# Kernel tuning notes

Measured on AMD Instinct MI355X. Metric: run time of the kernel, lower is better.

The kernel has to match this reference:

```python
import jax, jax.numpy as jnp
import numpy as np

N_NODES = 50000
HIDDEN = 128
N_EDGES = 1_600_000


def gcn_conv(x, W, b, src, dst, n_nodes):
    """PyG GCNConv: linear, add self-loops, symmetric deg^-1/2 normalization, scatter-sum."""
    h = x @ W  # [N, D]
    # degree with self-loops: 1 + in-degree from edges (edge weight 1)
    deg = jnp.ones((n_nodes,), h.dtype).at[dst].add(1.0)
    dinv = jax.lax.rsqrt(deg)  # deg^{-1/2}, deg >= 1 so no inf
    # neighbor messages: norm_e = dinv[src] * dinv[dst]
    msgs = h[src] * (dinv[src] * dinv[dst])[:, None]  # [E, D]
    agg = jnp.zeros_like(h).at[dst].add(msgs)
    # self-loop contribution: norm = dinv[i]*dinv[i]
    agg = agg + h * (dinv * dinv)[:, None]
    return agg + b


def setup_inputs() -> dict:
    key = jax.random.key(0)
    ks = jax.random.split(key, 7)
    x = jax.random.normal(ks[0], (N_NODES, HIDDEN), dtype=jnp.float32)
    edge_index = jax.random.randint(ks[1], (2, N_EDGES), 0, N_NODES, dtype=jnp.int64)
    s = 1.0 / np.sqrt(HIDDEN)
    W1 = jax.random.uniform(ks[2], (HIDDEN, HIDDEN), jnp.float32, -s, s)
    b1 = jax.random.uniform(ks[3], (HIDDEN,), jnp.float32, -s, s)
    W2 = jax.random.uniform(ks[4], (HIDDEN, HIDDEN), jnp.float32, -s, s)
    b2 = jax.random.uniform(ks[5], (HIDDEN,), jnp.float32, -s, s)
    return {"x": x, "edge_index": edge_index, "W1": W1, "b1": b1, "W2": W2, "b2": b2}


def reference(x, edge_index, W1, b1, W2, b2):
    src, dst = edge_index[0], edge_index[1]
    h = jax.nn.relu(gcn_conv(x, W1, b1, src, dst, N_NODES))
    z = gcn_conv(h, W2, b2, src, dst, N_NODES)
    return z
```

## Files before the change

kernel.cpp:

```cpp
#include <hip/hip_runtime.h>
#include <hip/hip_fp16.h>
#include <type_traits>

#define D 128
#define NI 128
#define NR 25000


__global__ __launch_bounds__(1024) void histA_kernel(const int* __restrict__ dst,
                                                     int* __restrict__ c,
                                                     int E, int N, int CH) {
  __shared__ int cnt[NR];
  int i = blockIdx.x, r = blockIdx.y;
  int base = r * NR;
  int kmax = min(NR, N - base);
  for (int k = threadIdx.x; k < kmax; k += 1024) cnt[k] = 0;
  __syncthreads();
  int e0 = i * CH, e1 = min(e0 + CH, E);
  for (int e = e0 + (int)threadIdx.x; e < e1; e += 1024) {
    unsigned dr = (unsigned)(dst[e] - base);
    if (dr < (unsigned)kmax) atomicAdd(&cnt[dr], 1);
  }
  __syncthreads();
  int* ci = c + (size_t)i * N + base;
  for (int k = threadIdx.x; k < kmax; k += 1024) ci[k] = cnt[k];
}


__global__ __launch_bounds__(256) void histB_kernel(int* __restrict__ c,
                                                    int* __restrict__ deg, int N) {
  int n = blockIdx.x * 256 + threadIdx.x;
  if (n >= N) return;
  int run = 0;
  #pragma unroll 8
  for (int i = 0; i < NI; ++i) {
    size_t idx = (size_t)i * N + n;
    int v = c[idx];
    c[idx] = run;
    run += v;
  }
  deg[n] = run;
}


__global__ __launch_bounds__(256) void bsum_kernel(const int* __restrict__ deg,
                                                   int* __restrict__ bsum) {
  __shared__ int ws[4];
  int i0 = blockIdx.x * 1024 + threadIdx.x * 4;
  int4 v = *reinterpret_cast<const int4*>(deg + i0);
  int s = v.x + v.y + v.z + v.w;
  #pragma unroll
  for (int off = 32; off; off >>= 1) s += __shfl_down(s, off);
  if ((threadIdx.x & 63) == 0) ws[threadIdx.x >> 6] = s;
  __syncthreads();
  if (threadIdx.x == 0) bsum[blockIdx.x] = ws[0] + ws[1] + ws[2] + ws[3];
}


__global__ __launch_bounds__(256) void scan_kernel(const int* __restrict__ deg,
                                                   const int* __restrict__ bsum,
                                                   int* __restrict__ offsets,
                                                   float* __restrict__ dinv,
                                                   int N, int E) {
  __shared__ int ts[256];
  int b = blockIdx.x;
  int base = 0;
  for (int t = 0; t < b; ++t) base += bsum[t];

  int i0 = b * 1024 + threadIdx.x * 4;
  int4 v = *reinterpret_cast<const int4*>(deg + i0);
  int t4 = v.x + v.y + v.z + v.w;
  ts[threadIdx.x] = t4;
  __syncthreads();
  #pragma unroll
  for (int off = 1; off < 256; off <<= 1) {
    int u = (threadIdx.x >= off) ? ts[threadIdx.x - off] : 0;
    __syncthreads();
    ts[threadIdx.x] += u;
    __syncthreads();
  }
  int run = base + ts[threadIdx.x] - t4;

  int dd[4] = {v.x, v.y, v.z, v.w};
  #pragma unroll
  for (int k = 0; k < 4; ++k) {
    int i = i0 + k;
    if (i < N) {
      offsets[i] = run;
      dinv[i] = rsqrtf(1.0f + (float)dd[k]);
    }
    run += dd[k];
  }
  if (b == 0 && threadIdx.x == 0) offsets[N] = E;
}


__global__ __launch_bounds__(1024) void placeC_kernel(const int* __restrict__ src,
                                                      const int* __restrict__ dst,
                                                      const int* __restrict__ c,
                                                      const int* __restrict__ offsets,
                                                      const float* __restrict__ dinv,
                                                      unsigned int* __restrict__ csr,
                                                      int E, int N, int CH) {
  __shared__ int cnt[NR];
  int i = blockIdx.x, r = blockIdx.y;
  int base = r * NR;
  int kmax = min(NR, N - base);
  const int* ci = c + (size_t)i * N + base;
  for (int k = threadIdx.x; k < kmax; k += 1024) cnt[k] = offsets[base + k] + ci[k];
  __syncthreads();
  int e0 = i * CH, e1 = min(e0 + CH, E);
  for (int e = e0 + (int)threadIdx.x; e < e1; e += 1024) {
    int d = dst[e];
    unsigned dr = (unsigned)(d - base);
    if (dr < (unsigned)kmax) {
      int pos = atomicAdd(&cnt[dr], 1);
      int s = src[e];
      float nm = dinv[s] * dinv[d];
      unsigned int q = (unsigned int)__float2int_rn(nm * 32767.0f);
      csr[pos] = ((unsigned int)s << 15) | q;
    }
  }
}


template <typename TI>
__global__ __launch_bounds__(256) void gemm_kernel(const TI* __restrict__ X,
                                                   const float* __restrict__ W,
                                                   __half* __restrict__ H, int N) {
  __shared__ float xs[32 * D];
  int row0 = blockIdx.x * 32;
  if constexpr (std::is_same<TI, float>::value) {
    #pragma unroll
    for (int jj = 0; jj < 4; ++jj) {
      int f4 = threadIdx.x + jj * 256;
      int r = f4 >> 5;
      float4 v = make_float4(0.f, 0.f, 0.f, 0.f);
      if (row0 + r < N) v = *reinterpret_cast<const float4*>(X + (size_t)row0 * D + (size_t)f4 * 4);
      *reinterpret_cast<float4*>(xs + f4 * 4) = v;
    }
  } else {
    #pragma unroll
    for (int jj = 0; jj < 2; ++jj) {
      int g8 = threadIdx.x + jj * 256;
      int r = g8 >> 4;
      uint4 raw = make_uint4(0u, 0u, 0u, 0u);
      if (row0 + r < N)
        raw = *reinterpret_cast<const uint4*>((const __half*)X + (size_t)row0 * D + (size_t)g8 * 8);
      const __half2* hp = reinterpret_cast<const __half2*>(&raw);
      float* dst8 = xs + (size_t)g8 * 8;
      #pragma unroll
      for (int k = 0; k < 4; ++k) {
        float2 f = __half22float2(hp[k]);
        dst8[k * 2] = f.x;
        dst8[k * 2 + 1] = f.y;
      }
    }
  }
  __syncthreads();

  int tx = threadIdx.x & 63;
  int ty = threadIdx.x >> 6;
  int c0 = tx * 2;
  float2 acc[8];
  #pragma unroll
  for (int r = 0; r < 8; ++r) acc[r] = make_float2(0.f, 0.f);
  const float* xbase = xs + ty * 8 * D;

  for (int k = 0; k < D; k += 4) {
    float2 w0 = *reinterpret_cast<const float2*>(W + (size_t)(k + 0) * D + c0);
    float2 w1 = *reinterpret_cast<const float2*>(W + (size_t)(k + 1) * D + c0);
    float2 w2 = *reinterpret_cast<const float2*>(W + (size_t)(k + 2) * D + c0);
    float2 w3 = *reinterpret_cast<const float2*>(W + (size_t)(k + 3) * D + c0);
    #pragma unroll
    for (int r = 0; r < 8; ++r) {
      float4 xv = *reinterpret_cast<const float4*>(xbase + r * D + k);
      acc[r].x = fmaf(xv.x, w0.x, acc[r].x); acc[r].y = fmaf(xv.x, w0.y, acc[r].y);
      acc[r].x = fmaf(xv.y, w1.x, acc[r].x); acc[r].y = fmaf(xv.y, w1.y, acc[r].y);
      acc[r].x = fmaf(xv.z, w2.x, acc[r].x); acc[r].y = fmaf(xv.z, w2.y, acc[r].y);
      acc[r].x = fmaf(xv.w, w3.x, acc[r].x); acc[r].y = fmaf(xv.w, w3.y, acc[r].y);
    }
  }

  #pragma unroll
  for (int r = 0; r < 8; ++r) {
    int row = row0 + ty * 8 + r;
    if (row < N)
      *reinterpret_cast<__half2*>(H + (size_t)row * D + c0) = __floats2half2_rn(acc[r].x, acc[r].y);
  }
}


template <int DO_RELU, typename TO>
__global__ __launch_bounds__(256) void agg_kernel(const __half* __restrict__ H,
                                                  const int* __restrict__ offsets,
                                                  const unsigned int* __restrict__ csr,
                                                  const float* __restrict__ dinv,
                                                  const float* __restrict__ bias,
                                                  TO* __restrict__ out, int N) {
  int n = blockIdx.x * 4 + (threadIdx.x >> 6);
  if (n >= N) return;
  int lane = threadIdx.x & 63;
  int g = lane >> 4;
  int l = lane & 15;

  int beg = offsets[n];
  int end = offsets[n + 1];

  float acc[8];
  #pragma unroll
  for (int k = 0; k < 8; ++k) acc[k] = 0.f;

  const __half* Hl = H + l * 8;

  int j = beg + g;
  for (; j + 12 < end; j += 16) {
    unsigned int p0 = csr[j];
    unsigned int p1 = csr[j + 4];
    unsigned int p2 = csr[j + 8];
    unsigned int p3 = csr[j + 12];
    float m0 = (float)(p0 & 0x7fffu) * (1.0f / 32767.0f);
    float m1 = (float)(p1 & 0x7fffu) * (1.0f / 32767.0f);
    float m2 = (float)(p2 & 0x7fffu) * (1.0f / 32767.0f);
    float m3 = (float)(p3 & 0x7fffu) * (1.0f / 32767.0f);
    uint4 r0 = *reinterpret_cast<const uint4*>(Hl + (size_t)(p0 >> 15) * D);
    uint4 r1 = *reinterpret_cast<const uint4*>(Hl + (size_t)(p1 >> 15) * D);
    uint4 r2 = *reinterpret_cast<const uint4*>(Hl + (size_t)(p2 >> 15) * D);
    uint4 r3 = *reinterpret_cast<const uint4*>(Hl + (size_t)(p3 >> 15) * D);
    const __half2* h0 = reinterpret_cast<const __half2*>(&r0);
    const __half2* h1 = reinterpret_cast<const __half2*>(&r1);
    const __half2* h2 = reinterpret_cast<const __half2*>(&r2);
    const __half2* h3 = reinterpret_cast<const __half2*>(&r3);
    #pragma unroll
    for (int k = 0; k < 4; ++k) {
      float2 f0 = __half22float2(h0[k]);
      float2 f1 = __half22float2(h1[k]);
      float2 f2 = __half22float2(h2[k]);
      float2 f3 = __half22float2(h3[k]);
      acc[2 * k]     = fmaf(f0.x, m0, acc[2 * k]);
      acc[2 * k + 1] = fmaf(f0.y, m0, acc[2 * k + 1]);
      acc[2 * k]     = fmaf(f1.x, m1, acc[2 * k]);
      acc[2 * k + 1] = fmaf(f1.y, m1, acc[2 * k + 1]);
      acc[2 * k]     = fmaf(f2.x, m2, acc[2 * k]);
      acc[2 * k + 1] = fmaf(f2.y, m2, acc[2 * k + 1]);
      acc[2 * k]     = fmaf(f3.x, m3, acc[2 * k]);
      acc[2 * k + 1] = fmaf(f3.y, m3, acc[2 * k + 1]);
    }
  }
  for (; j < end; j += 4) {
    unsigned int p0 = csr[j];
    float m0 = (float)(p0 & 0x7fffu) * (1.0f / 32767.0f);
    uint4 r0 = *reinterpret_cast<const uint4*>(Hl + (size_t)(p0 >> 15) * D);
    const __half2* h0 = reinterpret_cast<const __half2*>(&r0);
    #pragma unroll
    for (int k = 0; k < 4; ++k) {
      float2 f0 = __half22float2(h0[k]);
      acc[2 * k]     = fmaf(f0.x, m0, acc[2 * k]);
      acc[2 * k + 1] = fmaf(f0.y, m0, acc[2 * k + 1]);
    }
  }

  #pragma unroll
  for (int k = 0; k < 8; ++k) {
    acc[k] += __shfl_xor(acc[k], 16);
    acc[k] += __shfl_xor(acc[k], 32);
  }

  if (g == 0) {
    float di = dinv[n];
    float dii = di * di;
    uint4 rs = *reinterpret_cast<const uint4*>(Hl + (size_t)n * D);
    const __half2* hs = reinterpret_cast<const __half2*>(&rs);
    float4 bv0 = *reinterpret_cast<const float4*>(bias + l * 8);
    float4 bv1 = *reinterpret_cast<const float4*>(bias + l * 8 + 4);
    float v[8];
    #pragma unroll
    for (int k = 0; k < 4; ++k) {
      float2 f = __half22float2(hs[k]);
      v[2 * k]     = fmaf(f.x, dii, acc[2 * k]);
      v[2 * k + 1] = fmaf(f.y, dii, acc[2 * k + 1]);
    }
    v[0] += bv0.x; v[1] += bv0.y; v[2] += bv0.z; v[3] += bv0.w;
    v[4] += bv1.x; v[5] += bv1.y; v[6] += bv1.z; v[7] += bv1.w;
    if (DO_RELU) {
      #pragma unroll
      for (int k = 0; k < 8; ++k) v[k] = fmaxf(v[k], 0.f);
    }
    if constexpr (std::is_same<TO, float>::value) {
      float4 o0 = make_float4(v[0], v[1], v[2], v[3]);
      float4 o1 = make_float4(v[4], v[5], v[6], v[7]);
      *reinterpret_cast<float4*>(out + (size_t)n * D + l * 8) = o0;
      *reinterpret_cast<float4*>(out + (size_t)n * D + l * 8 + 4) = o1;
    } else {
      uint4 pk;
      __half2 q0 = __floats2half2_rn(v[0], v[1]);
      __half2 q1 = __floats2half2_rn(v[2], v[3]);
      __half2 q2 = __floats2half2_rn(v[4], v[5]);
      __half2 q3 = __floats2half2_rn(v[6], v[7]);
      pk.x = *reinterpret_cast<unsigned int*>(&q0);
      pk.y = *reinterpret_cast<unsigned int*>(&q1);
      pk.z = *reinterpret_cast<unsigned int*>(&q2);
      pk.w = *reinterpret_cast<unsigned int*>(&q3);
      *reinterpret_cast<uint4*>((__half*)out + (size_t)n * D + l * 8) = pk;
    }
  }
}


extern "C" void kernel_launch(void* const* d_in, const int* in_sizes, int n_in,
                              void* d_out, int out_size, void* d_ws, size_t ws_size,
                              hipStream_t stream) {
  const float* x  = (const float*)d_in[0];
  const int* edge = (const int*)d_in[1];
  const float* W1 = (const float*)d_in[2];
  const float* b1 = (const float*)d_in[3];
  const float* W2 = (const float*)d_in[4];
  const float* b2 = (const float*)d_in[5];
  const int N = in_sizes[0] / D;
  const int E = in_sizes[1] / 2;
  const int* srcp = edge;
  const int* dstp = edge + E;
  float* out = (float*)d_out;

  const int NP = (N + 1023) & ~1023;
  const int SB = NP / 1024;
  const int CH = (E + NI - 1) / NI;
  const int NRB = (N + NR - 1) / NR;

  auto align = [](size_t v) { return (v + 255) & ~(size_t)255; };
  char* ws = (char*)d_ws;
  size_t o = 0;
  int*   deg     = (int*)(ws + o);             o += align((size_t)NP * 4);
  int*   bsum    = (int*)(ws + o);             o += align((size_t)SB * 4);
  int*   offsets = (int*)(ws + o);             o += align((size_t)(N + 1) * 4);
  float* dinv    = (float*)(ws + o);           o += align((size_t)N * 4);
  int*   c       = (int*)(ws + o);             o += align((size_t)NI * N * 4);
  unsigned int* csr = (unsigned int*)(ws + o); o += align((size_t)E * 4);
  __half* Hh     = (__half*)(ws + o);          o += align((size_t)N * D * 2);
  __half* h1h    = (__half*)(ws + o);          o += align((size_t)N * D * 2);

  int gemm_blocks = (N + 31) / 32;
  int agg_blocks  = (N + 3) / 4;

  hipMemsetAsync(deg, 0, (size_t)NP * 4, stream);
  histA_kernel<<<dim3(NI, NRB), 1024, 0, stream>>>(dstp, c, E, N, CH);
  histB_kernel<<<(N + 255) / 256, 256, 0, stream>>>(c, deg, N);
  bsum_kernel<<<SB, 256, 0, stream>>>(deg, bsum);
  scan_kernel<<<SB, 256, 0, stream>>>(deg, bsum, offsets, dinv, N, E);
  placeC_kernel<<<dim3(NI, NRB), 1024, 0, stream>>>(srcp, dstp, c, offsets, dinv, csr, E, N, CH);

  gemm_kernel<float><<<gemm_blocks, 256, 0, stream>>>(x, W1, Hh, N);
  agg_kernel<1, __half><<<agg_blocks, 256, 0, stream>>>(Hh, offsets, csr, dinv, b1, h1h, N);

  gemm_kernel<__half><<<gemm_blocks, 256, 0, stream>>>(h1h, W2, Hh, N);
  agg_kernel<0, float><<<agg_blocks, 256, 0, stream>>>(Hh, offsets, csr, dinv, b2, out, N);
}
```

Baseline: 241.2 us.

## Use MFMA fp16 GEMM with pre-transposed weights and 16-bit histogram counters

Replaces the scalar-FMA shared-memory GEMM with an MFMA 16x16x32 f16 kernel. Each wave loads its A rows straight into registers and reads a transposed fp16 copy of W, which a small new prep kernel builds. Separately, the per-chunk histogram count array shrinks from int to unsigned short, halving its traffic in histA, histB and placeC. The risks are fp16 rounding of x and W before the multiply, and overflow of the 16-bit prefix counts if a single node has more than 65535 incoming edges.

```diff
diff --git a/kernel.cpp b/kernel.cpp
--- a/kernel.cpp
+++ b/kernel.cpp
@@ -6,9 +6,25 @@
 #define NI 128
 #define NR 25000
 
+using half8 = __attribute__((ext_vector_type(8))) _Float16;
+using f32x4 = __attribute__((ext_vector_type(4))) float;
+
+
+__global__ __launch_bounds__(256) void wprep_kernel(const float* __restrict__ W1,
+                                                    const float* __restrict__ W2,
+                                                    __half* __restrict__ Wt1,
+                                                    __half* __restrict__ Wt2) {
+  const float* W = blockIdx.x ? W2 : W1;
+  __half* Wt = blockIdx.x ? Wt2 : Wt1;
+  for (int idx = threadIdx.x; idx < D * D; idx += 256) {
+    int c = idx & 127, k = idx >> 7;
+    Wt[c * D + k] = __float2half(W[k * D + c]);
+  }
+}
+
 
 __global__ __launch_bounds__(1024) void histA_kernel(const int* __restrict__ dst,
-                                                     int* __restrict__ c,
+                                                     unsigned short* __restrict__ c,
                                                      int E, int N, int CH) {
   __shared__ int cnt[NR];
   int i = blockIdx.x, r = blockIdx.y;
@@ -22,12 +38,12 @@
     if (dr < (unsigned)kmax) atomicAdd(&cnt[dr], 1);
   }
   __syncthreads();
-  int* ci = c + (size_t)i * N + base;
-  for (int k = threadIdx.x; k < kmax; k += 1024) ci[k] = cnt[k];
-}
-
-
-__global__ __launch_bounds__(256) void histB_kernel(int* __restrict__ c,
+  unsigned short* ci = c + (size_t)i * N + base;
+  for (int k = threadIdx.x; k < kmax; k += 1024) ci[k] = (unsigned short)cnt[k];
+}
+
+
+__global__ __launch_bounds__(256) void histB_kernel(unsigned short* __restrict__ c,
                                                     int* __restrict__ deg, int N) {
   int n = blockIdx.x * 256 + threadIdx.x;
   if (n >= N) return;
@@ -36,7 +52,7 @@
   for (int i = 0; i < NI; ++i) {
     size_t idx = (size_t)i * N + n;
     int v = c[idx];
-    c[idx] = run;
+    c[idx] = (unsigned short)run;
     run += v;
   }
   deg[n] = run;
@@ -97,7 +113,7 @@
 
 __global__ __launch_bounds__(1024) void placeC_kernel(const int* __restrict__ src,
                                                       const int* __restrict__ dst,
-                                                      const int* __restrict__ c,
+                                                      const unsigned short* __restrict__ c,
                                                       const int* __restrict__ offsets,
                                                       const float* __restrict__ dinv,
                                                       unsigned int* __restrict__ csr,
@@ -106,8 +122,8 @@
   int i = blockIdx.x, r = blockIdx.y;
   int base = r * NR;
   int kmax = min(NR, N - base);
-  const int* ci = c + (size_t)i * N + base;
-  for (int k = threadIdx.x; k < kmax; k += 1024) cnt[k] = offsets[base + k] + ci[k];
+  const unsigned short* ci = c + (size_t)i * N + base;
+  for (int k = threadIdx.x; k < kmax; k += 1024) cnt[k] = offsets[base + k] + (int)ci[k];
   __syncthreads();
   int e0 = i * CH, e1 = min(e0 + CH, E);
   for (int e = e0 + (int)threadIdx.x; e < e1; e += 1024) {
@@ -125,68 +141,50 @@
 
 
 template <typename TI>
-__global__ __launch_bounds__(256) void gemm_kernel(const TI* __restrict__ X,
-                                                   const float* __restrict__ W,
-                                                   __half* __restrict__ H, int N) {
-  __shared__ float xs[32 * D];
-  int row0 = blockIdx.x * 32;
-  if constexpr (std::is_same<TI, float>::value) {
-    #pragma unroll
-    for (int jj = 0; jj < 4; ++jj) {
-      int f4 = threadIdx.x + jj * 256;
-      int r = f4 >> 5;
-      float4 v = make_float4(0.f, 0.f, 0.f, 0.f);
-      if (row0 + r < N) v = *reinterpret_cast<const float4*>(X + (size_t)row0 * D + (size_t)f4 * 4);
-      *reinterpret_cast<float4*>(xs + f4 * 4) = v;
-    }
-  } else {
-    #pragma unroll
-    for (int jj = 0; jj < 2; ++jj) {
-      int g8 = threadIdx.x + jj * 256;
-      int r = g8 >> 4;
-      uint4 raw = make_uint4(0u, 0u, 0u, 0u);
-      if (row0 + r < N)
-        raw = *reinterpret_cast<const uint4*>((const __half*)X + (size_t)row0 * D + (size_t)g8 * 8);
-      const __half2* hp = reinterpret_cast<const __half2*>(&raw);
-      float* dst8 = xs + (size_t)g8 * 8;
-      #pragma unroll
-      for (int k = 0; k < 4; ++k) {
-        float2 f = __half22float2(hp[k]);
-        dst8[k * 2] = f.x;
-        dst8[k * 2 + 1] = f.y;
+__global__ __launch_bounds__(256) void gemm_mfma_kernel(const TI* __restrict__ X,
+                                                        const __half* __restrict__ Wt,
+                                                        __half* __restrict__ H, int N) {
+  int wid = threadIdx.x >> 6;
+  int l = threadIdx.x & 63;
+  int row0w = blockIdx.x * 64 + wid * 16;
+  int arow = row0w + (l & 15);
+  int k0 = (l >> 4) * 8;
+
+  half8 A[4];
+  #pragma unroll
+  for (int kt = 0; kt < 4; ++kt) {
+    half8 a = {};
+    if (arow < N) {
+      if constexpr (std::is_same<TI, float>::value) {
+        const float* p = X + (size_t)arow * D + kt * 32 + k0;
+        float4 u = *reinterpret_cast<const float4*>(p);
+        float4 v = *reinterpret_cast<const float4*>(p + 4);
+        a[0] = (_Float16)u.x; a[1] = (_Float16)u.y;
+        a[2] = (_Float16)u.z; a[3] = (_Float16)u.w;
+        a[4] = (_Float16)v.x; a[5] = (_Float16)v.y;
+        a[6] = (_Float16)v.z; a[7] = (_Float16)v.w;
+      } else {
+        a = *reinterpret_cast<const half8*>((const __half*)X + (size_t)arow * D + kt * 32 + k0);
       }
     }
-  }
-  __syncthreads();
-
-  int tx = threadIdx.x & 63;
-  int ty = threadIdx.x >> 6;
-  int c0 = tx * 2;
-  float2 acc[8];
-  #pragma unroll
-  for (int r = 0; r < 8; ++r) acc[r] = make_float2(0.f, 0.f);
-  const float* xbase = xs + ty * 8 * D;
-
-  for (int k = 0; k < D; k += 4) {
-    float2 w0 = *reinterpret_cast<const float2*>(W + (size_t)(k + 0) * D + c0);
-    float2 w1 = *reinterpret_cast<const float2*>(W + (size_t)(k + 1) * D + c0);
-    float2 w2 = *reinterpret_cast<const float2*>(W + (size_t)(k + 2) * D + c0);
-    float2 w3 = *reinterpret_cast<const float2*>(W + (size_t)(k + 3) * D + c0);
-    #pragma unroll
-    for (int r = 0; r < 8; ++r) {
-      float4 xv = *reinterpret_cast<const float4*>(xbase + r * D + k);
-      acc[r].x = fmaf(xv.x, w0.x, acc[r].x); acc[r].y = fmaf(xv.x, w0.y, acc[r].y);
-      acc[r].x = fmaf(xv.y, w1.x, acc[r].x); acc[r].y = fmaf(xv.y, w1.y, acc[r].y);
-      acc[r].x = fmaf(xv.z, w2.x, acc[r].x); acc[r].y = fmaf(xv.z, w2.y, acc[r].y);
-      acc[r].x = fmaf(xv.w, w3.x, acc[r].x); acc[r].y = fmaf(xv.w, w3.y, acc[r].y);
-    }
-  }
-
-  #pragma unroll
-  for (int r = 0; r < 8; ++r) {
-    int row = row0 + ty * 8 + r;
-    if (row < N)
-      *reinterpret_cast<__half2*>(H + (size_t)row * D + c0) = __floats2half2_rn(acc[r].x, acc[r].y);
+    A[kt] = a;
+  }
+
+  int wrow = row0w + (l >> 4) * 4;
+  int col = l & 15;
+  #pragma unroll
+  for (int ct = 0; ct < 8; ++ct) {
+    f32x4 acc = {0.f, 0.f, 0.f, 0.f};
+    #pragma unroll
+    for (int kt = 0; kt < 4; ++kt) {
+      half8 b = *reinterpret_cast<const half8*>(Wt + (size_t)(ct * 16 + col) * D + kt * 32 + k0);
+      acc = __builtin_amdgcn_mfma_f32_16x16x32_f16(A[kt], b, acc, 0, 0, 0);
+    }
+    #pragma unroll
+    for (int r = 0; r < 4; ++r) {
+      int row = wrow + r;
+      if (row < N) H[(size_t)row * D + ct * 16 + col] = __float2half(acc[r]);
+    }
   }
 }
 
@@ -334,24 +332,27 @@
   int*   bsum    = (int*)(ws + o);             o += align((size_t)SB * 4);
   int*   offsets = (int*)(ws + o);             o += align((size_t)(N + 1) * 4);
   float* dinv    = (float*)(ws + o);           o += align((size_t)N * 4);
-  int*   c       = (int*)(ws + o);             o += align((size_t)NI * N * 4);
+  unsigned short* c = (unsigned short*)(ws + o); o += align((size_t)NI * N * 2);
   unsigned int* csr = (unsigned int*)(ws + o); o += align((size_t)E * 4);
   __half* Hh     = (__half*)(ws + o);          o += align((size_t)N * D * 2);
   __half* h1h    = (__half*)(ws + o);          o += align((size_t)N * D * 2);
-
-  int gemm_blocks = (N + 31) / 32;
+  __half* Wt1    = (__half*)(ws + o);          o += align((size_t)D * D * 2);
+  __half* Wt2    = (__half*)(ws + o);          o += align((size_t)D * D * 2);
+
+  int gemm_blocks = (N + 63) / 64;
   int agg_blocks  = (N + 3) / 4;
 
   hipMemsetAsync(deg, 0, (size_t)NP * 4, stream);
+  wprep_kernel<<<2, 256, 0, stream>>>(W1, W2, Wt1, Wt2);
   histA_kernel<<<dim3(NI, NRB), 1024, 0, stream>>>(dstp, c, E, N, CH);
   histB_kernel<<<(N + 255) / 256, 256, 0, stream>>>(c, deg, N);
   bsum_kernel<<<SB, 256, 0, stream>>>(deg, bsum);
   scan_kernel<<<SB, 256, 0, stream>>>(deg, bsum, offsets, dinv, N, E);
   placeC_kernel<<<dim3(NI, NRB), 1024, 0, stream>>>(srcp, dstp, c, offsets, dinv, csr, E, N, CH);
 
-  gemm_kernel<float><<<gemm_blocks, 256, 0, stream>>>(x, W1, Hh, N);
+  gemm_mfma_kernel<float><<<gemm_blocks, 256, 0, stream>>>(x, Wt1, Hh, N);
   agg_kernel<1, __half><<<agg_blocks, 256, 0, stream>>>(Hh, offsets, csr, dinv, b1, h1h, N);
 
-  gemm_kernel<__half><<<gemm_blocks, 256, 0, stream>>>(h1h, W2, Hh, N);
+  gemm_mfma_kernel<__half><<<gemm_blocks, 256, 0, stream>>>(h1h, Wt2, Hh, N);
   agg_kernel<0, float><<<agg_blocks, 256, 0, stream>>>(Hh, offsets, csr, dinv, b2, out, N);
 }
```

New measurement: 233.0 us (median of 2 runs). -3.4%, faster.
